# Kernel tuning notes

Measured on AMD Instinct MI355X. Metric: run time of the kernel, lower is better.

The kernel has to match this reference:

```python
import jax, jax.numpy as jnp
import numpy as np

NEG_SLOPE = 0.2  # PyG GATConv default

def gat_conv(x, src, dst, W, att_src, att_dst, bias, n_nodes):
    """PyG-style GATConv (self-loops already included in src/dst)."""
    H, C = att_src.shape
    h = (x @ W).reshape(n_nodes, H, C)                       # [N,H,C]
    a_src = jnp.einsum('nhc,hc->nh', h, att_src)             # [N,H]
    a_dst = jnp.einsum('nhc,hc->nh', h, att_dst)             # [N,H]
    e = jax.nn.leaky_relu(a_src[src] + a_dst[dst], NEG_SLOPE)  # [E,H]
    # numerically stable segment softmax over incoming edges of each dst node
    e_max = jax.ops.segment_max(e, dst, num_segments=n_nodes)   # [N,H]
    e_exp = jnp.exp(e - e_max[dst])
    denom = jax.ops.segment_sum(e_exp, dst, num_segments=n_nodes)  # [N,H]
    alpha = e_exp / (denom[dst] + 1e-16)                     # [E,H]
    msg = h[src] * alpha[:, :, None]                         # [E,H,C]
    out = jax.ops.segment_sum(msg, dst, num_segments=n_nodes)  # [N,H,C]
    return out.reshape(n_nodes, H * C) + bias

def add_self_loops(edge_index, n_nodes):
    loop = jnp.arange(n_nodes, dtype=edge_index.dtype)
    src = jnp.concatenate([edge_index[0], loop])
    dst = jnp.concatenate([edge_index[1], loop])
    return src, dst

def setup_inputs() -> dict:
    key = jax.random.key(0)
    ks = jax.random.split(key, 12)
    N, E, IN, HID, H1 = 50000, 800000, 128, 64, 4
    s = lambda k, shape, scale: jax.random.normal(k, shape, dtype=jnp.float32) * scale
    return {
        'x': s(ks[0], (N, IN), 1.0),
        'edge_index': jax.random.randint(ks[1], (2, E), 0, N, dtype=jnp.int64),
        'W1': s(ks[2], (IN, H1 * HID), (2.0 / IN) ** 0.5),
        'att_src1': s(ks[3], (H1, HID), 0.1),
        'att_dst1': s(ks[4], (H1, HID), 0.1),
        'b1': s(ks[5], (H1 * HID,), 0.02),
        'W2': s(ks[6], (H1 * HID, HID), (2.0 / (H1 * HID)) ** 0.5),
        'att_src2': s(ks[7], (1, HID), 0.1),
        'att_dst2': s(ks[8], (1, HID), 0.1),
        'b2': s(ks[9], (HID,), 0.02),
        'Ws': s(ks[10], (HID, 1), (2.0 / HID) ** 0.5),
        'bs': s(ks[11], (1,), 0.02),
    }

def reference(x, edge_index, W1, att_src1, att_dst1, b1, W2, att_src2, att_dst2, b2, Ws, bs):
    N = x.shape[0]
    src, dst = add_self_loops(edge_index, N)
    h = jax.nn.elu(gat_conv(x, src, dst, W1, att_src1, att_dst1, b1, N))   # [N,256]
    # dropout is identity in eval mode
    h = jax.nn.elu(gat_conv(h, src, dst, W2, att_src2, att_dst2, b2, N))   # [N,64]
    scores = (h @ Ws + bs).squeeze(-1)                                     # [N]
    return h, scores
```

## Files before the change

kernel.cpp:

```cpp
#include <hip/hip_runtime.h>
#include <hip/hip_bf16.h>
#include <math.h>


#define LRELU_SLOPE 0.2f

typedef __attribute__((ext_vector_type(8))) short short8;
typedef __attribute__((ext_vector_type(4))) float f32x4;

__device__ inline ushort f2bf(float f) {
    uint u = __float_as_uint(f);
    return (ushort)((u + 0x7FFFu + ((u >> 16) & 1u)) >> 16);
}
__device__ inline float bf2f(ushort u) {
    return __uint_as_float(((uint)u) << 16);
}

__device__ inline void prefrag_one(const float* __restrict__ W,
                                   ushort* __restrict__ out,
                                   int tid, int T, int ldn)
{
    int l = tid & 63, jt = tid >> 6;
    int t = jt % T, j = jt / T;
    int n = j * 16 + (l & 15);
    int k0 = t * 32 + (l >> 4) * 8;
    ushort o[8];
    #pragma unroll
    for (int b = 0; b < 8; ++b) o[b] = f2bf(W[(size_t)(k0 + b) * ldn + n]);
    *(short8*)(out + (size_t)tid * 8) = *(short8*)o;
}

__global__ __launch_bounds__(256)
void fused_front(const float* __restrict__ x, ushort* __restrict__ xbf,
                 const float* __restrict__ W1, const float* __restrict__ W2,
                 ushort* __restrict__ o1, ushort* __restrict__ o2,
                 const int* __restrict__ edst, int* __restrict__ deg,
                 int* __restrict__ order, int nconv4, int E)
{
    int tid = blockIdx.x * blockDim.x + threadIdx.x;
    if (tid < nconv4) {
        int i = tid << 2;
        float4 v = *(const float4*)(x + i);
        ushort4 o;
        o.x = f2bf(v.x); o.y = f2bf(v.y); o.z = f2bf(v.z); o.w = f2bf(v.w);
        *(ushort4*)(xbf + i) = o;
        return;
    }
    int t = tid - nconv4;
    if (t < 16 * 4 * 64) { prefrag_one(W1, o1, t, 4, 256); return; }
    t -= 16 * 4 * 64;
    if (t < 4 * 8 * 64)  { prefrag_one(W2, o2, t, 8, 64); return; }
    t -= 4 * 8 * 64;
    int i = t << 2;
    if (i + 3 < E) {
        int4 v = *(const int4*)(edst + i);
        int4 o;
        o.x = atomicAdd(&deg[v.x], 1);
        o.y = atomicAdd(&deg[v.y], 1);
        o.z = atomicAdd(&deg[v.z], 1);
        o.w = atomicAdd(&deg[v.w], 1);
        *(int4*)(order + i) = o;
    } else {
        for (; i < E; ++i) order[i] = atomicAdd(&deg[edst[i]], 1);
    }
}

__global__ __launch_bounds__(1024)
void scan_rowptr(const int* __restrict__ deg, int* __restrict__ rowptr, int N)
{
    __shared__ int wsums[16];
    const int tid = threadIdx.x, lane = tid & 63, wid = tid >> 6;
    const int N4 = N >> 2;
    const int b4 = tid * 13;
    int tsum = 0;
    #pragma unroll
    for (int k = 0; k < 13; ++k) {
        int i4 = b4 + k;
        if (i4 < N4) {
            int4 v = ((const int4*)deg)[i4];
            tsum += (v.x + v.y) + (v.z + v.w);
        }
    }
    int sc = tsum;
    #pragma unroll
    for (int off = 1; off < 64; off <<= 1) {
        int t = __shfl_up(sc, off);
        if (lane >= off) sc += t;
    }
    if (lane == 63) wsums[wid] = sc;
    __syncthreads();
    if (wid == 0) {
        int wv = (lane < 16) ? wsums[lane] : 0;
        #pragma unroll
        for (int off = 1; off < 16; off <<= 1) {
            int t = __shfl_up(wv, off);
            if (lane >= off) wv += t;
        }
        if (lane < 16) wsums[lane] = wv;
    }
    __syncthreads();
    int run = (wid ? wsums[wid - 1] : 0) + sc - tsum;
    #pragma unroll
    for (int k = 0; k < 13; ++k) {
        int i4 = b4 + k;
        if (i4 < N4) {
            int4 v = ((const int4*)deg)[i4];
            int4 o;
            o.x = run; o.y = run + v.x; o.z = o.y + v.y; o.w = o.z + v.z;
            ((int4*)rowptr)[i4] = o;
            run += (v.x + v.y) + (v.z + v.w);
        }
    }
    if (tid == 1023) rowptr[N] = run;
}

template<int J, int T, int H>
__device__ inline void gemm_body(int wid, const ushort* __restrict__ A,
                                 const ushort* __restrict__ Bf,
                                 ushort* __restrict__ Cbf,
                                 const float* __restrict__ attS,
                                 const float* __restrict__ attD,
                                 float* __restrict__ as_,
                                 float* __restrict__ ad_, int M)
{
    constexpr int K = 32 * T;
    constexpr int NN = 16 * J;
    const int l = threadIdx.x & 63;
    const int base = wid * 16;
    if (base >= M) return;
    const int lm = l & 15, lg = l >> 4;

    short8 a[T];
    const ushort* ap = A + (size_t)(base + lm) * K + lg * 8;
    #pragma unroll
    for (int t = 0; t < T; ++t) a[t] = *(const short8*)(ap + t * 32);

    f32x4 acc[J];
    #pragma unroll
    for (int j = 0; j < J; ++j) acc[j] = (f32x4){0.f, 0.f, 0.f, 0.f};

    const ushort* bp = Bf + (size_t)l * 8;
    #pragma unroll
    for (int j = 0; j < J; ++j)
        #pragma unroll
        for (int t = 0; t < T; ++t) {
            short8 b = *(const short8*)(bp + (size_t)(j * T + t) * 512);
            acc[j] = __builtin_amdgcn_mfma_f32_16x16x32_bf16(a[t], b, acc[j], 0, 0, 0);
        }

    float sp[H][4], dp[H][4];
    #pragma unroll
    for (int h = 0; h < H; ++h)
        #pragma unroll
        for (int r = 0; r < 4; ++r) { sp[h][r] = 0.f; dp[h][r] = 0.f; }

    #pragma unroll
    for (int j = 0; j < J; ++j) {
        const int h = j / (J / H);
        const int coff = (j % (J / H)) * 16 + lm;
        float ws = attS[h * 64 + coff];
        float wd = attD[h * 64 + coff];
        #pragma unroll
        for (int r = 0; r < 4; ++r) {
            int row = base + lg * 4 + r;
            Cbf[(size_t)row * NN + j * 16 + lm] = f2bf(acc[j][r]);
            sp[h][r] = fmaf(acc[j][r], ws, sp[h][r]);
            dp[h][r] = fmaf(acc[j][r], wd, dp[h][r]);
        }
    }
    #pragma unroll
    for (int h = 0; h < H; ++h)
        #pragma unroll
        for (int r = 0; r < 4; ++r) {
            float s = sp[h][r], d = dp[h][r];
            s += __shfl_xor(s, 1); d += __shfl_xor(d, 1);
            s += __shfl_xor(s, 2); d += __shfl_xor(d, 2);
            s += __shfl_xor(s, 4); d += __shfl_xor(d, 4);
            s += __shfl_xor(s, 8); d += __shfl_xor(d, 8);
            if (lm == 0) {
                int row = base + lg * 4 + r;
                as_[row * H + h] = s;
                ad_[row * H + h] = d;
            }
        }
}

__global__ __launch_bounds__(256)
void scatter_gemm1(const ushort* __restrict__ A, const ushort* __restrict__ Bf,
                   ushort* __restrict__ Cbf, const float* __restrict__ attS,
                   const float* __restrict__ attD, float* __restrict__ as_,
                   float* __restrict__ ad_, int M, int gemmBlocks,
                   const int* __restrict__ esrc, const int* __restrict__ edst,
                   const int* __restrict__ rowptr, const int* __restrict__ order,
                   int* __restrict__ csr_src, int E)
{
    if ((int)blockIdx.x < gemmBlocks) {
        int wid = blockIdx.x * (blockDim.x >> 6) + (threadIdx.x >> 6);
        gemm_body<16, 4, 4>(wid, A, Bf, Cbf, attS, attD, as_, ad_, M);
        return;
    }
    int i = (blockIdx.x - gemmBlocks) * blockDim.x + threadIdx.x;
    if (i >= E) return;
    csr_src[rowptr[edst[i]] + order[i]] = esrc[i];
}

template<int J, int T, int H>
__global__ __launch_bounds__(256)
void gemm_mfma(const ushort* __restrict__ A, const ushort* __restrict__ Bf,
               ushort* __restrict__ Cbf, const float* __restrict__ attS,
               const float* __restrict__ attD, float* __restrict__ as_,
               float* __restrict__ ad_, int M)
{
    int wid = blockIdx.x * (blockDim.x >> 6) + (threadIdx.x >> 6);
    gemm_body<J, T, H>(wid, A, Bf, Cbf, attS, attD, as_, ad_, M);
}

__global__ __launch_bounds__(256)
void aggregate_l1(const int* __restrict__ rowptr, const int* __restrict__ csr_src,
                  const ushort* __restrict__ h1, const float* __restrict__ as_,
                  const float* __restrict__ ad_, const float* __restrict__ bias,
                  ushort* __restrict__ outbf, int N)
{
    int w = (blockIdx.x * blockDim.x + threadIdx.x) >> 6;
    int lane = threadIdx.x & 63;
    if (w >= N) return;
    const int head = lane >> 4;
    const int c0 = lane << 2;
    const int my = lane & 3;
    const int hb = lane & 48;
    const float ad = ad_[w * 4 + head];
    float4 acc;
    float dsum;

    {
        float el = as_[w * 4 + head] + ad;
        el = el > 0.f ? el : LRELU_SLOPE * el;
        float p = __expf(el);
        ushort4 u = *(const ushort4*)(h1 + (size_t)w * 256 + c0);
        acc.x = p * bf2f(u.x); acc.y = p * bf2f(u.y);
        acc.z = p * bf2f(u.z); acc.w = p * bf2f(u.w);
        dsum = p;
    }

    int e = rowptr[w];
    const int e1 = rowptr[w + 1];
    for (; e + 3 < e1; e += 4) {
        int s0 = csr_src[e],     s1 = csr_src[e + 1];
        int s2 = csr_src[e + 2], s3 = csr_src[e + 3];
        ushort4 u0 = *(const ushort4*)(h1 + (size_t)s0 * 256 + c0);
        ushort4 u1 = *(const ushort4*)(h1 + (size_t)s1 * 256 + c0);
        ushort4 u2 = *(const ushort4*)(h1 + (size_t)s2 * 256 + c0);
        ushort4 u3 = *(const ushort4*)(h1 + (size_t)s3 * 256 + c0);
        int ms = s0;
        ms = (my == 1) ? s1 : ms;
        ms = (my == 2) ? s2 : ms;
        ms = (my == 3) ? s3 : ms;
        float ev = as_[ms * 4 + head] + ad;
        ev = ev > 0.f ? ev : LRELU_SLOPE * ev;
        float pl = __expf(ev);
        float p0 = __shfl(pl, hb | 0);
        float p1 = __shfl(pl, hb | 1);
        float p2 = __shfl(pl, hb | 2);
        float p3 = __shfl(pl, hb | 3);
        acc.x = fmaf(p0, bf2f(u0.x), acc.x); acc.y = fmaf(p0, bf2f(u0.y), acc.y);
        acc.z = fmaf(p0, bf2f(u0.z), acc.z); acc.w = fmaf(p0, bf2f(u0.w), acc.w);
        acc.x = fmaf(p1, bf2f(u1.x), acc.x); acc.y = fmaf(p1, bf2f(u1.y), acc.y);
        acc.z = fmaf(p1, bf2f(u1.z), acc.z); acc.w = fmaf(p1, bf2f(u1.w), acc.w);
        acc.x = fmaf(p2, bf2f(u2.x), acc.x); acc.y = fmaf(p2, bf2f(u2.y), acc.y);
        acc.z = fmaf(p2, bf2f(u2.z), acc.z); acc.w = fmaf(p2, bf2f(u2.w), acc.w);
        acc.x = fmaf(p3, bf2f(u3.x), acc.x); acc.y = fmaf(p3, bf2f(u3.y), acc.y);
        acc.z = fmaf(p3, bf2f(u3.z), acc.z); acc.w = fmaf(p3, bf2f(u3.w), acc.w);
        dsum += (p0 + p1) + (p2 + p3);
    }
    for (; e < e1; ++e) {
        int s0 = csr_src[e];
        float e0 = as_[s0 * 4 + head] + ad;
        e0 = e0 > 0.f ? e0 : LRELU_SLOPE * e0;
        float p0 = __expf(e0);
        ushort4 u0 = *(const ushort4*)(h1 + (size_t)s0 * 256 + c0);
        acc.x = fmaf(p0, bf2f(u0.x), acc.x); acc.y = fmaf(p0, bf2f(u0.y), acc.y);
        acc.z = fmaf(p0, bf2f(u0.z), acc.z); acc.w = fmaf(p0, bf2f(u0.w), acc.w);
        dsum += p0;
    }
    const float inv = 1.f / (dsum + 1e-16f);
    const float4 b = *(const float4*)(bias + c0);
    float ox = acc.x * inv + b.x; ox = ox > 0.f ? ox : expm1f(ox);
    float oy = acc.y * inv + b.y; oy = oy > 0.f ? oy : expm1f(oy);
    float oz = acc.z * inv + b.z; oz = oz > 0.f ? oz : expm1f(oz);
    float ow = acc.w * inv + b.w; ow = ow > 0.f ? ow : expm1f(ow);
    ushort4 o;
    o.x = f2bf(ox); o.y = f2bf(oy); o.z = f2bf(oz); o.w = f2bf(ow);
    *(ushort4*)(outbf + (size_t)w * 256 + c0) = o;
}

__global__ __launch_bounds__(256)
void aggregate_l2(const int* __restrict__ rowptr, const int* __restrict__ csr_src,
                  const ushort* __restrict__ h2, const float* __restrict__ as_,
                  const float* __restrict__ ad_, const float* __restrict__ b2,
                  const float* __restrict__ Wsv, const float* __restrict__ bs,
                  float* __restrict__ hout, float* __restrict__ scores, int N)
{
    int w = (blockIdx.x * blockDim.x + threadIdx.x) >> 6;
    int lane = threadIdx.x & 63;
    if (w >= N) return;
    const int my = lane & 3;
    const float ad = ad_[w];
    float acc, dsum;
    {
        float el = as_[w] + ad;
        el = el > 0.f ? el : LRELU_SLOPE * el;
        float p = __expf(el);
        acc = p * bf2f(h2[(size_t)w * 64 + lane]);
        dsum = p;
    }
    int e = rowptr[w];
    const int e1 = rowptr[w + 1];
    for (; e + 3 < e1; e += 4) {
        int s0 = csr_src[e],     s1 = csr_src[e + 1];
        int s2 = csr_src[e + 2], s3 = csr_src[e + 3];
        ushort f0 = h2[(size_t)s0 * 64 + lane];
        ushort f1 = h2[(size_t)s1 * 64 + lane];
        ushort f2 = h2[(size_t)s2 * 64 + lane];
        ushort f3 = h2[(size_t)s3 * 64 + lane];
        int ms = s0;
        ms = (my == 1) ? s1 : ms;
        ms = (my == 2) ? s2 : ms;
        ms = (my == 3) ? s3 : ms;
        float ev = as_[ms] + ad;
        ev = ev > 0.f ? ev : LRELU_SLOPE * ev;
        float pl = __expf(ev);
        float p0 = __shfl(pl, 0);
        float p1 = __shfl(pl, 1);
        float p2 = __shfl(pl, 2);
        float p3 = __shfl(pl, 3);
        acc = fmaf(p0, bf2f(f0), acc);
        acc = fmaf(p1, bf2f(f1), acc);
        acc = fmaf(p2, bf2f(f2), acc);
        acc = fmaf(p3, bf2f(f3), acc);
        dsum += (p0 + p1) + (p2 + p3);
    }
    for (; e < e1; ++e) {
        int s0 = csr_src[e];
        float e0 = as_[s0] + ad;
        e0 = e0 > 0.f ? e0 : LRELU_SLOPE * e0;
        float p0 = __expf(e0);
        acc = fmaf(p0, bf2f(h2[(size_t)s0 * 64 + lane]), acc);
        dsum += p0;
    }
    float v = acc / (dsum + 1e-16f) + b2[lane];
    v = v > 0.f ? v : expm1f(v);
    hout[(size_t)w * 64 + lane] = v;
    float sc = v * Wsv[lane];
    #pragma unroll
    for (int off = 32; off; off >>= 1) sc += __shfl_down(sc, off);
    if (lane == 0) scores[w] = sc + bs[0];
}

extern "C" void kernel_launch(void* const* d_in, const int* in_sizes, int n_in,
                              void* d_out, int out_size, void* d_ws, size_t ws_size,
                              hipStream_t stream)
{
    const float* x    = (const float*)d_in[0];
    const int*   ei   = (const int*)d_in[1];
    const float* W1   = (const float*)d_in[2];
    const float* as1w = (const float*)d_in[3];
    const float* ad1w = (const float*)d_in[4];
    const float* b1   = (const float*)d_in[5];
    const float* W2   = (const float*)d_in[6];
    const float* as2w = (const float*)d_in[7];
    const float* ad2w = (const float*)d_in[8];
    const float* b2   = (const float*)d_in[9];
    const float* Ws   = (const float*)d_in[10];
    const float* bs   = (const float*)d_in[11];

    const int N  = in_sizes[0] / 128;
    const int E  = in_sizes[1] / 2;
    const int* esrc = ei;
    const int* edst = ei + E;

    ushort* h1bf  = (ushort*)d_ws;
    ushort* hl1bf = h1bf + (size_t)N * 256;
    ushort* h2bf  = hl1bf + (size_t)N * 256;
    ushort* xbf   = h2bf + (size_t)N * 64;
    ushort* bfr1  = xbf + (size_t)N * 128;
    ushort* bfr2  = bfr1 + 32768;
    float*  as1   = (float*)(bfr2 + 16384);
    float*  ad1   = as1 + (size_t)N * 4;
    float*  as2   = ad1 + (size_t)N * 4;
    float*  ad2   = as2 + N;
    int*    deg    = (int*)(ad2 + N);
    int*    order  = deg + N;
    int*    rowptr = order + E;
    int*    csr_src= rowptr + N + 4;

    float* hout   = (float*)d_out;
    float* scores = hout + (size_t)N * 64;

    hipMemsetAsync(deg, 0, (size_t)N * sizeof(int), stream);

    const int nconv4 = N * 128 / 4;
    const int nfrag  = 16 * 4 * 64 + 4 * 8 * 64;
    const int nhist  = (E + 3) / 4;
    fused_front<<<(nconv4 + nfrag + nhist + 255) / 256, 256, 0, stream>>>(
        x, xbf, W1, W2, bfr1, bfr2, edst, deg, order, nconv4, E);

    scan_rowptr<<<1, 1024, 0, stream>>>(deg, rowptr, N);

    const int gemmBlocks    = (N / 16 + 3) / 4;
    const int scatterBlocks = (E + 255) / 256;
    scatter_gemm1<<<gemmBlocks + scatterBlocks, 256, 0, stream>>>(
        xbf, bfr1, h1bf, as1w, ad1w, as1, ad1, N, gemmBlocks,
        esrc, edst, rowptr, order, csr_src, E);

    aggregate_l1<<<((size_t)N * 64 + 255) / 256, 256, 0, stream>>>(
        rowptr, csr_src, h1bf, as1, ad1, b1, hl1bf, N);

    gemm_mfma<4, 8, 1><<<(N / 16 + 3) / 4, 256, 0, stream>>>(
        hl1bf, bfr2, h2bf, as2w, ad2w, as2, ad2, N);

    aggregate_l2<<<((size_t)N * 64 + 255) / 256, 256, 0, stream>>>(
        rowptr, csr_src, h2bf, as2, ad2, b2, Ws, bs, hout, scores, N);
}
```

Measured before the change: 226.7 us.

## Split layer-2 aggregation wave into four edge-parallel quarters with vectorized loads

```diff
diff --git a/kernel.cpp b/kernel.cpp
--- a/kernel.cpp
+++ b/kernel.cpp
@@ -303,56 +303,64 @@
     int w = (blockIdx.x * blockDim.x + threadIdx.x) >> 6;
     int lane = threadIdx.x & 63;
     if (w >= N) return;
-    const int my = lane & 3;
+    const int q  = lane >> 4;
+    const int ql = lane & 15;
+    const int c0 = ql << 2;
     const float ad = ad_[w];
-    float acc, dsum;
+
+    float acc[4];
+    float dsum;
     {
         float el = as_[w] + ad;
         el = el > 0.f ? el : LRELU_SLOPE * el;
-        float p = __expf(el);
-        acc = p * bf2f(h2[(size_t)w * 64 + lane]);
+        float p = (q == 0) ? __expf(el) : 0.f;
+        ushort4 u = *(const ushort4*)(h2 + (size_t)w * 64 + c0);
+        acc[0] = p * bf2f(u.x); acc[1] = p * bf2f(u.y);
+        acc[2] = p * bf2f(u.z); acc[3] = p * bf2f(u.w);
         dsum = p;
     }
+
     int e = rowptr[w];
     const int e1 = rowptr[w + 1];
-    for (; e + 3 < e1; e += 4) {
-        int s0 = csr_src[e],     s1 = csr_src[e + 1];
-        int s2 = csr_src[e + 2], s3 = csr_src[e + 3];
-        ushort f0 = h2[(size_t)s0 * 64 + lane];
-        ushort f1 = h2[(size_t)s1 * 64 + lane];
-        ushort f2 = h2[(size_t)s2 * 64 + lane];
-        ushort f3 = h2[(size_t)s3 * 64 + lane];
-        int ms = s0;
-        ms = (my == 1) ? s1 : ms;
-        ms = (my == 2) ? s2 : ms;
-        ms = (my == 3) ? s3 : ms;
-        float ev = as_[ms] + ad;
-        ev = ev > 0.f ? ev : LRELU_SLOPE * ev;
-        float pl = __expf(ev);
-        float p0 = __shfl(pl, 0);
-        float p1 = __shfl(pl, 1);
-        float p2 = __shfl(pl, 2);
-        float p3 = __shfl(pl, 3);
-        acc = fmaf(p0, bf2f(f0), acc);
-        acc = fmaf(p1, bf2f(f1), acc);
-        acc = fmaf(p2, bf2f(f2), acc);
-        acc = fmaf(p3, bf2f(f3), acc);
-        dsum += (p0 + p1) + (p2 + p3);
-    }
-    for (; e < e1; ++e) {
-        int s0 = csr_src[e];
-        float e0 = as_[s0] + ad;
-        e0 = e0 > 0.f ? e0 : LRELU_SLOPE * e0;
-        float p0 = __expf(e0);
-        acc = fmaf(p0, bf2f(h2[(size_t)s0 * 64 + lane]), acc);
-        dsum += p0;
-    }
-    float v = acc / (dsum + 1e-16f) + b2[lane];
-    v = v > 0.f ? v : expm1f(v);
-    hout[(size_t)w * 64 + lane] = v;
-    float sc = v * Wsv[lane];
-    #pragma unroll
-    for (int off = 32; off; off >>= 1) sc += __shfl_down(sc, off);
+    const int eL = e1 - 1;
+    while (e < e1) {
+        #pragma unroll
+        for (int u2 = 0; u2 < 2; ++u2) {
+            int m = e + 4 * u2 + q;
+            int idx = m <= eL ? m : eL;
+            int s = csr_src[idx];
+            float ev = as_[s] + ad;
+            ev = ev > 0.f ? ev : LRELU_SLOPE * ev;
+            float p = m <= eL ? __expf(ev) : 0.f;
+            ushort4 u = *(const ushort4*)(h2 + (size_t)s * 64 + c0);
+            acc[0] = fmaf(p, bf2f(u.x), acc[0]);
+            acc[1] = fmaf(p, bf2f(u.y), acc[1]);
+            acc[2] = fmaf(p, bf2f(u.z), acc[2]);
+            acc[3] = fmaf(p, bf2f(u.w), acc[3]);
+            dsum += p;
+        }
+        e += 8;
+    }
+
+    dsum += __shfl_xor(dsum, 16); dsum += __shfl_xor(dsum, 32);
+    #pragma unroll
+    for (int k = 0; k < 4; ++k) {
+        acc[k] += __shfl_xor(acc[k], 16);
+        acc[k] += __shfl_xor(acc[k], 32);
+    }
+
+    const float inv = 1.f / (dsum + 1e-16f);
+    const float4 bb = *(const float4*)(b2 + c0);
+    const float4 ww = *(const float4*)(Wsv + c0);
+    float v0 = acc[0] * inv + bb.x; v0 = v0 > 0.f ? v0 : expm1f(v0);
+    float v1 = acc[1] * inv + bb.y; v1 = v1 > 0.f ? v1 : expm1f(v1);
+    float v2 = acc[2] * inv + bb.z; v2 = v2 > 0.f ? v2 : expm1f(v2);
+    float v3 = acc[3] * inv + bb.w; v3 = v3 > 0.f ? v3 : expm1f(v3);
+    if (q == 0)
+        *(float4*)(hout + (size_t)w * 64 + c0) = make_float4(v0, v1, v2, v3);
+    float sc = fmaf(v0, ww.x, fmaf(v1, ww.y, fmaf(v2, ww.z, v3 * ww.w)));
+    sc += __shfl_xor(sc, 1); sc += __shfl_xor(sc, 2);
+    sc += __shfl_xor(sc, 4); sc += __shfl_xor(sc, 8);
     if (lane == 0) scores[w] = sc + bs[0];
 }
 
```

Measured after the change: 228.3 us. Within noise of the previous version (+0.7%).

## Fuse layer-1 aggregation with layer-2 GEMM via shared-memory tile

Applied to the files above, without the earlier changes.

```diff
diff --git a/kernel.cpp b/kernel.cpp
--- a/kernel.cpp
+++ b/kernel.cpp
@@ -204,93 +204,137 @@
     csr_src[rowptr[edst[i]] + order[i]] = esrc[i];
 }
 
-template<int J, int T, int H>
 __global__ __launch_bounds__(256)
-void gemm_mfma(const ushort* __restrict__ A, const ushort* __restrict__ Bf,
-               ushort* __restrict__ Cbf, const float* __restrict__ attS,
-               const float* __restrict__ attD, float* __restrict__ as_,
-               float* __restrict__ ad_, int M)
-{
-    int wid = blockIdx.x * (blockDim.x >> 6) + (threadIdx.x >> 6);
-    gemm_body<J, T, H>(wid, A, Bf, Cbf, attS, attD, as_, ad_, M);
-}
-
-__global__ __launch_bounds__(256)
-void aggregate_l1(const int* __restrict__ rowptr, const int* __restrict__ csr_src,
-                  const ushort* __restrict__ h1, const float* __restrict__ as_,
-                  const float* __restrict__ ad_, const float* __restrict__ bias,
-                  ushort* __restrict__ outbf, int N)
-{
-    int w = (blockIdx.x * blockDim.x + threadIdx.x) >> 6;
-    int lane = threadIdx.x & 63;
-    if (w >= N) return;
+void agg1_gemm2(const int* __restrict__ rowptr, const int* __restrict__ csr_src,
+                const ushort* __restrict__ h1, const float* __restrict__ as_,
+                const float* __restrict__ ad_, const float* __restrict__ bias,
+                const ushort* __restrict__ Bf2, const float* __restrict__ attS2,
+                const float* __restrict__ attD2, float* __restrict__ as2,
+                float* __restrict__ ad2, ushort* __restrict__ h2bf, int N)
+{
+    __shared__ ushort hl[16][264];
+    __shared__ float partS[4][16], partD[4][16];
+    const int lane = threadIdx.x & 63;
+    const int v = threadIdx.x >> 6;
+    const int nbase = blockIdx.x * 16;
     const int head = lane >> 4;
     const int c0 = lane << 2;
     const int my = lane & 3;
     const int hb = lane & 48;
-    const float ad = ad_[w * 4 + head];
-    float4 acc;
-    float dsum;
+
+    for (int qn = 0; qn < 4; ++qn) {
+        const int w = nbase + v * 4 + qn;
+        if (w >= N) break;
+        const float ad = ad_[w * 4 + head];
+        float4 acc;
+        float dsum;
+        {
+            float el = as_[w * 4 + head] + ad;
+            el = el > 0.f ? el : LRELU_SLOPE * el;
+            float p = __expf(el);
+            ushort4 u = *(const ushort4*)(h1 + (size_t)w * 256 + c0);
+            acc.x = p * bf2f(u.x); acc.y = p * bf2f(u.y);
+            acc.z = p * bf2f(u.z); acc.w = p * bf2f(u.w);
+            dsum = p;
+        }
+        int e = rowptr[w];
+        const int e1 = rowptr[w + 1];
+        for (; e + 3 < e1; e += 4) {
+            int s0 = csr_src[e],     s1 = csr_src[e + 1];
+            int s2 = csr_src[e + 2], s3 = csr_src[e + 3];
+            ushort4 u0 = *(const ushort4*)(h1 + (size_t)s0 * 256 + c0);
+            ushort4 u1 = *(const ushort4*)(h1 + (size_t)s1 * 256 + c0);
+            ushort4 u2 = *(const ushort4*)(h1 + (size_t)s2 * 256 + c0);
+            ushort4 u3 = *(const ushort4*)(h1 + (size_t)s3 * 256 + c0);
+            int ms = s0;
+            ms = (my == 1) ? s1 : ms;
+            ms = (my == 2) ? s2 : ms;
+            ms = (my == 3) ? s3 : ms;
+            float ev = as_[ms * 4 + head] + ad;
+            ev = ev > 0.f ? ev : LRELU_SLOPE * ev;
+            float pl = __expf(ev);
+            float p0 = __shfl(pl, hb | 0);
+            float p1 = __shfl(pl, hb | 1);
+            float p2 = __shfl(pl, hb | 2);
+            float p3 = __shfl(pl, hb | 3);
+            acc.x = fmaf(p0, bf2f(u0.x), acc.x); acc.y = fmaf(p0, bf2f(u0.y), acc.y);
+            acc.z = fmaf(p0, bf2f(u0.z), acc.z); acc.w = fmaf(p0, bf2f(u0.w), acc.w);
+            acc.x = fmaf(p1, bf2f(u1.x), acc.x); acc.y = fmaf(p1, bf2f(u1.y), acc.y);
+            acc.z = fmaf(p1, bf2f(u1.z), acc.z); acc.w = fmaf(p1, bf2f(u1.w), acc.w);
+            acc.x = fmaf(p2, bf2f(u2.x), acc.x); acc.y = fmaf(p2, bf2f(u2.y), acc.y);
+            acc.z = fmaf(p2, bf2f(u2.z), acc.z); acc.w = fmaf(p2, bf2f(u2.w), acc.w);
+            acc.x = fmaf(p3, bf2f(u3.x), acc.x); acc.y = fmaf(p3, bf2f(u3.y), acc.y);
+            acc.z = fmaf(p3, bf2f(u3.z), acc.z); acc.w = fmaf(p3, bf2f(u3.w), acc.w);
+            dsum += (p0 + p1) + (p2 + p3);
+        }
+        for (; e < e1; ++e) {
+            int s0 = csr_src[e];
+            float e0 = as_[s0 * 4 + head] + ad;
+            e0 = e0 > 0.f ? e0 : LRELU_SLOPE * e0;
+            float p0 = __expf(e0);
+            ushort4 u0 = *(const ushort4*)(h1 + (size_t)s0 * 256 + c0);
+            acc.x = fmaf(p0, bf2f(u0.x), acc.x); acc.y = fmaf(p0, bf2f(u0.y), acc.y);
+            acc.z = fmaf(p0, bf2f(u0.z), acc.z); acc.w = fmaf(p0, bf2f(u0.w), acc.w);
+            dsum += p0;
+        }
+        const float inv = 1.f / (dsum + 1e-16f);
+        const float4 b = *(const float4*)(bias + c0);
+        float ox = acc.x * inv + b.x; ox = ox > 0.f ? ox : expm1f(ox);
+        float oy = acc.y * inv + b.y; oy = oy > 0.f ? oy : expm1f(oy);
+        float oz = acc.z * inv + b.z; oz = oz > 0.f ? oz : expm1f(oz);
+        float ow = acc.w * inv + b.w; ow = ow > 0.f ? ow : expm1f(ow);
+        ushort4 o;
+        o.x = f2bf(ox); o.y = f2bf(oy); o.z = f2bf(oz); o.w = f2bf(ow);
+        *(ushort4*)&hl[v * 4 + qn][c0] = o;
+    }
+    __syncthreads();
 
     {
-        float el = as_[w * 4 + head] + ad;
-        el = el > 0.f ? el : LRELU_SLOPE * el;
-        float p = __expf(el);
-        ushort4 u = *(const ushort4*)(h1 + (size_t)w * 256 + c0);
-        acc.x = p * bf2f(u.x); acc.y = p * bf2f(u.y);
-        acc.z = p * bf2f(u.z); acc.w = p * bf2f(u.w);
-        dsum = p;
-    }
-
-    int e = rowptr[w];
-    const int e1 = rowptr[w + 1];
-    for (; e + 3 < e1; e += 4) {
-        int s0 = csr_src[e],     s1 = csr_src[e + 1];
-        int s2 = csr_src[e + 2], s3 = csr_src[e + 3];
-        ushort4 u0 = *(const ushort4*)(h1 + (size_t)s0 * 256 + c0);
-        ushort4 u1 = *(const ushort4*)(h1 + (size_t)s1 * 256 + c0);
-        ushort4 u2 = *(const ushort4*)(h1 + (size_t)s2 * 256 + c0);
-        ushort4 u3 = *(const ushort4*)(h1 + (size_t)s3 * 256 + c0);
-        int ms = s0;
-        ms = (my == 1) ? s1 : ms;
-        ms = (my == 2) ? s2 : ms;
-        ms = (my == 3) ? s3 : ms;
-        float ev = as_[ms * 4 + head] + ad;
-        ev = ev > 0.f ? ev : LRELU_SLOPE * ev;
-        float pl = __expf(ev);
-        float p0 = __shfl(pl, hb | 0);
-        float p1 = __shfl(pl, hb | 1);
-        float p2 = __shfl(pl, hb | 2);
-        float p3 = __shfl(pl, hb | 3);
-        acc.x = fmaf(p0, bf2f(u0.x), acc.x); acc.y = fmaf(p0, bf2f(u0.y), acc.y);
-        acc.z = fmaf(p0, bf2f(u0.z), acc.z); acc.w = fmaf(p0, bf2f(u0.w), acc.w);
-        acc.x = fmaf(p1, bf2f(u1.x), acc.x); acc.y = fmaf(p1, bf2f(u1.y), acc.y);
-        acc.z = fmaf(p1, bf2f(u1.z), acc.z); acc.w = fmaf(p1, bf2f(u1.w), acc.w);
-        acc.x = fmaf(p2, bf2f(u2.x), acc.x); acc.y = fmaf(p2, bf2f(u2.y), acc.y);
-        acc.z = fmaf(p2, bf2f(u2.z), acc.z); acc.w = fmaf(p2, bf2f(u2.w), acc.w);
-        acc.x = fmaf(p3, bf2f(u3.x), acc.x); acc.y = fmaf(p3, bf2f(u3.y), acc.y);
-        acc.z = fmaf(p3, bf2f(u3.z), acc.z); acc.w = fmaf(p3, bf2f(u3.w), acc.w);
-        dsum += (p0 + p1) + (p2 + p3);
-    }
-    for (; e < e1; ++e) {
-        int s0 = csr_src[e];
-        float e0 = as_[s0 * 4 + head] + ad;
-        e0 = e0 > 0.f ? e0 : LRELU_SLOPE * e0;
-        float p0 = __expf(e0);
-        ushort4 u0 = *(const ushort4*)(h1 + (size_t)s0 * 256 + c0);
-        acc.x = fmaf(p0, bf2f(u0.x), acc.x); acc.y = fmaf(p0, bf2f(u0.y), acc.y);
-        acc.z = fmaf(p0, bf2f(u0.z), acc.z); acc.w = fmaf(p0, bf2f(u0.w), acc.w);
-        dsum += p0;
-    }
-    const float inv = 1.f / (dsum + 1e-16f);
-    const float4 b = *(const float4*)(bias + c0);
-    float ox = acc.x * inv + b.x; ox = ox > 0.f ? ox : expm1f(ox);
-    float oy = acc.y * inv + b.y; oy = oy > 0.f ? oy : expm1f(oy);
-    float oz = acc.z * inv + b.z; oz = oz > 0.f ? oz : expm1f(oz);
-    float ow = acc.w * inv + b.w; ow = ow > 0.f ? ow : expm1f(ow);
-    ushort4 o;
-    o.x = f2bf(ox); o.y = f2bf(oy); o.z = f2bf(oz); o.w = f2bf(ow);
-    *(ushort4*)(outbf + (size_t)w * 256 + c0) = o;
+        const int lm = lane & 15, lg = lane >> 4;
+        short8 a[8];
+        #pragma unroll
+        for (int t = 0; t < 8; ++t)
+            a[t] = *(const short8*)&hl[lm][lg * 8 + t * 32];
+        f32x4 acc = (f32x4){0.f, 0.f, 0.f, 0.f};
+        const ushort* bp = Bf2 + (size_t)(v * 8) * 512 + (size_t)lane * 8;
+        #pragma unroll
+        for (int t = 0; t < 8; ++t) {
+            short8 b = *(const short8*)(bp + (size_t)t * 512);
+            acc = __builtin_amdgcn_mfma_f32_16x16x32_bf16(a[t], b, acc, 0, 0, 0);
+        }
+        const float ws = attS2[v * 16 + lm];
+        const float wd = attD2[v * 16 + lm];
+        float sp[4], dp[4];
+        #pragma unroll
+        for (int r = 0; r < 4; ++r) {
+            int row = nbase + lg * 4 + r;
+            if (row < N)
+                h2bf[(size_t)row * 64 + v * 16 + lm] = f2bf(acc[r]);
+            sp[r] = acc[r] * ws;
+            dp[r] = acc[r] * wd;
+        }
+        #pragma unroll
+        for (int r = 0; r < 4; ++r) {
+            float s = sp[r], d = dp[r];
+            s += __shfl_xor(s, 1); d += __shfl_xor(d, 1);
+            s += __shfl_xor(s, 2); d += __shfl_xor(d, 2);
+            s += __shfl_xor(s, 4); d += __shfl_xor(d, 4);
+            s += __shfl_xor(s, 8); d += __shfl_xor(d, 8);
+            if (lm == 0) {
+                partS[v][lg * 4 + r] = s;
+                partD[v][lg * 4 + r] = d;
+            }
+        }
+    }
+    __syncthreads();
+    if (threadIdx.x < 16) {
+        int row = nbase + threadIdx.x;
+        if (row < N) {
+            int t = threadIdx.x;
+            as2[row] = ((partS[0][t] + partS[1][t]) + (partS[2][t] + partS[3][t]));
+            ad2[row] = ((partD[0][t] + partD[1][t]) + (partD[2][t] + partD[3][t]));
+        }
+    }
 }
 
 __global__ __launch_bounds__(256)
@@ -379,8 +423,7 @@
     const int* edst = ei + E;
 
     ushort* h1bf  = (ushort*)d_ws;
-    ushort* hl1bf = h1bf + (size_t)N * 256;
-    ushort* h2bf  = hl1bf + (size_t)N * 256;
+    ushort* h2bf  = h1bf + (size_t)N * 256;
     ushort* xbf   = h2bf + (size_t)N * 64;
     ushort* bfr1  = xbf + (size_t)N * 128;
     ushort* bfr2  = bfr1 + 32768;
@@ -412,11 +455,9 @@
         xbf, bfr1, h1bf, as1w, ad1w, as1, ad1, N, gemmBlocks,
         esrc, edst, rowptr, order, csr_src, E);
 
-    aggregate_l1<<<((size_t)N * 64 + 255) / 256, 256, 0, stream>>>(
-        rowptr, csr_src, h1bf, as1, ad1, b1, hl1bf, N);
-
-    gemm_mfma<4, 8, 1><<<(N / 16 + 3) / 4, 256, 0, stream>>>(
-        hl1bf, bfr2, h2bf, as2w, ad2w, as2, ad2, N);
+    agg1_gemm2<<<(N + 15) / 16, 256, 0, stream>>>(
+        rowptr, csr_src, h1bf, as1, ad1, b1,
+        bfr2, as2w, ad2w, as2, ad2, h2bf, N);
 
     aggregate_l2<<<((size_t)N * 64 + 255) / 256, 256, 0, stream>>>(
         rowptr, csr_src, h2bf, as2, ad2, b2, Ws, bs, hout, scores, N);
```

New measurement: 221.7 us. 2.2% less time.
